# Optimization experiments

Measured on AMD Instinct MI355X. Metric: run time of the kernel, lower is better.

The kernel has to match this reference:

```python
import jax, jax.numpy as jnp
import numpy as np

K = 16          # k_neighbours
BIG = 1e9       # distance penalty for masked senders


def setup_inputs() -> dict:
    key = jax.random.key(0)
    ks = jax.random.split(key, 8)
    B, N, F, H, FO = 64, 512, 64, 128, 64
    nodes = jax.random.normal(ks[0], (B, N, F), jnp.float32)
    mask = jax.random.randint(ks[1], (B, N), 0, 2, jnp.int32)

    def w(k_, sh):
        return jax.random.normal(k_, sh, jnp.float32) * (1.0 / np.sqrt(sh[0]).astype(np.float32))

    We1 = w(ks[2], (2 * F, H)); be1 = jnp.zeros((H,), jnp.float32)
    We2 = w(ks[3], (H, H));     be2 = jnp.zeros((H,), jnp.float32)
    Wn1 = w(ks[4], (F + H, H)); bn1 = jnp.zeros((H,), jnp.float32)
    Wn2 = w(ks[5], (H, FO));    bn2 = jnp.zeros((FO,), jnp.float32)
    return dict(nodes=nodes, mask=mask, We1=We1, be1=be1, We2=We2, be2=be2,
                Wn1=Wn1, bn1=bn1, Wn2=Wn2, bn2=bn2)


def reference(nodes, mask, We1, be1, We2, be2, Wn1, bn1, Wn2, bn2):
    # nodes: [B,N,F] ; mask: [B,N] (1 = real node, 0 = padding)
    m = mask.astype(nodes.dtype)                      # [B,N]
    x = nodes * m[..., None]                          # zero padded nodes

    # --- dynamic kNN graph (euclidean_squared + top_k, no self connection) ---
    sq = jnp.sum(x * x, axis=-1)                      # [B,N]
    dist = jnp.abs(sq[:, :, None] + sq[:, None, :]
                   - 2.0 * jnp.einsum('bnf,bmf->bnm', x, x))  # [B,N,N]
    dist = dist + BIG * (1.0 - m)[:, None, :]         # never select masked senders
    _, idx = jax.lax.top_k(-dist, K + 1)              # [B,N,K+1]
    idx = idx[..., 1:]                                # drop self connection -> [B,N,K]

    # --- gather sender features / masks along edges ---
    gathered = jax.vmap(lambda xf, ib: xf[ib])(x, idx)    # [B,N,K,F]
    smask = jax.vmap(lambda mv, ib: mv[ib])(m, idx)       # [B,N,K]
    recv = jnp.broadcast_to(x[:, :, None, :], gathered.shape)
    edges = jnp.concatenate([recv, gathered], axis=-1)    # [B,N,K,2F] ('concat' aggregation)

    # --- edge MLP (gather-compute) ---
    h = jax.nn.relu(edges @ We1 + be1)
    h = jax.nn.relu(h @ We2 + be2)                        # [B,N,K,H]

    # --- masked mean pooling over edges (scatter back to nodes) ---
    emask = m[:, :, None] * smask                         # edge valid iff both endpoints valid
    h = h * emask[..., None]
    cnt = jnp.maximum(jnp.sum(emask, axis=-1, keepdims=True), 1.0)  # [B,N,1]
    pooled = jnp.sum(h, axis=2) / cnt                     # [B,N,H]

    # --- node update MLP ---
    nh = jnp.concatenate([x, pooled], axis=-1)            # [B,N,F+H]
    out = jax.nn.relu(nh @ Wn1 + bn1) @ Wn2 + bn2         # [B,N,FO]
    return out * m[..., None]                             # zero padded nodes in output
```

## Files before the change

### kernel.cpp

```cpp
#include <hip/hip_runtime.h>

#define DI __device__ __forceinline__

typedef __bf16 bf16_t;
typedef __bf16 bf16x4 __attribute__((ext_vector_type(4)));
typedef __bf16 bf16x8 __attribute__((ext_vector_type(8)));
typedef float f32x4 __attribute__((ext_vector_type(4)));
typedef unsigned long long u64;


DI bf16_t f2b(float f) {
  unsigned u = __float_as_uint(f);
  unsigned r = (u + 0x7fffu + ((u >> 16) & 1u)) >> 16;
  return __builtin_bit_cast(bf16_t, (unsigned short)r);
}
DI float b2f(bf16_t h) {
  return __uint_as_float(((unsigned)__builtin_bit_cast(unsigned short, h)) << 16);
}
DI f32x4 zero4() { f32x4 z = {0.f, 0.f, 0.f, 0.f}; return z; }

DI bf16x8 make_frag(const float* p, bool wantlo) {
  float4 v0 = *(const float4*)p;
  float4 v1 = *(const float4*)(p + 4);
  float vv[8] = {v0.x, v0.y, v0.z, v0.w, v1.x, v1.y, v1.z, v1.w};
  bf16x8 a;
#pragma unroll
  for (int j = 0; j < 8; ++j) {
    bf16_t hi = f2b(vv[j]);
    a[j] = wantlo ? f2b(vv[j] - b2f(hi)) : hi;
  }
  return a;
}

DI u64 u64min(u64 a, u64 b) { return a < b ? a : b; }
template <int CTRL>
DI u64 dpp_u64(u64 v) {
  int lo = (int)(unsigned)(v & 0xffffffffull);
  int hi = (int)(unsigned)(v >> 32);
  int tlo = __builtin_amdgcn_update_dpp(0, lo, CTRL, 0xF, 0xF, true);
  int thi = __builtin_amdgcn_update_dpp(0, hi, CTRL, 0xF, 0xF, true);
  return (((u64)(unsigned)thi) << 32) | (unsigned)tlo;
}
template <int CTRL>
DI float dpp_f32(float v) {
  int t = __builtin_amdgcn_update_dpp(0, (int)__float_as_uint(v), CTRL, 0xF, 0xF, true);
  return __uint_as_float((unsigned)t);
}
DI u64 rowmin_u64(u64 v) {
  v = u64min(v, dpp_u64<0xB1>(v));
  v = u64min(v, dpp_u64<0x4E>(v));
  v = u64min(v, dpp_u64<0x141>(v));
  v = u64min(v, dpp_u64<0x140>(v));
  return v;
}
DI float rowsum_f32(float v) {
  v += dpp_f32<0xB1>(v);
  v += dpp_f32<0x4E>(v);
  v += dpp_f32<0x141>(v);
  v += dpp_f32<0x140>(v);
  return v;
}
DI void bitonic16(u64* a) {
#pragma unroll
  for (int k = 2; k <= 16; k <<= 1)
#pragma unroll
    for (int j = k >> 1; j > 0; j >>= 1)
#pragma unroll
      for (int i = 0; i < 16; ++i) {
        const int l = i ^ j;
        if (l > i) {
          const bool up = ((i & k) == 0);
          const bool sw = up ? (a[i] > a[l]) : (a[i] < a[l]);
          const u64 t0 = a[i], t1 = a[l];
          a[i] = sw ? t1 : t0;
          a[l] = sw ? t0 : t1;
        }
      }
}

__global__ void __launch_bounds__(256) kfuse(const float* __restrict__ nodes,
    const int* __restrict__ mask,
    const float* __restrict__ We1, const float* __restrict__ We2,
    const float* __restrict__ Wn1, const float* __restrict__ Wn2,
    float* __restrict__ x, bf16_t* __restrict__ xhi, bf16_t* __restrict__ xlo,
    float* __restrict__ sq, int* __restrict__ vlist, int* __restrict__ vcnt,
    bf16_t* __restrict__ W1p, bf16_t* __restrict__ W2p,
    bf16_t* __restrict__ Wn1p, bf16_t* __restrict__ Wn2p) {
  const int blk = blockIdx.x, t = threadIdx.x;
  __shared__ int cnts[8];
  __shared__ int basep[8];

  if (blk < 512) {
    const int b = blk >> 3, n0 = (blk & 7) * 64;
#pragma unroll
    for (int i = 0; i < 4; ++i) {
      const int idx = t + 256 * i;
      const int gi = b * 512 + n0 + (idx >> 4);
      const int fo = (idx & 15) * 4;
      const float fm = (float)mask[gi];
      const size_t ro = (size_t)gi * 64;
      float4 v = *(const float4*)(nodes + ro + fo);
      v.x *= fm; v.y *= fm; v.z *= fm; v.w *= fm;
      *(float4*)(x + ro + fo) = v;
      float vv[4] = {v.x, v.y, v.z, v.w};
      bf16x4 hh, ll;
#pragma unroll
      for (int k = 0; k < 4; ++k) {
        bf16_t hi = f2b(vv[k]);
        hh[k] = hi;
        ll[k] = f2b(vv[k] - b2f(hi));
      }
      *(bf16x4*)(xhi + ro + fo) = hh;
      *(bf16x4*)(xlo + ro + fo) = ll;
      float s = v.x * v.x + v.y * v.y + v.z * v.z + v.w * v.w;
      s = rowsum_f32(s);
      if ((t & 15) == 0) sq[gi] = s;
    }
  } else if (blk < 576) {
    const int b = blk - 512, lane = t & 63, w = t >> 6;
    unsigned long long bal[2]; int flag[2];
#pragma unroll
    for (int h = 0; h < 2; ++h) {
      flag[h] = (mask[b * 512 + h * 256 + t] != 0);
      bal[h] = __ballot(flag[h]);
      if (lane == 0) cnts[h * 4 + w] = __popcll(bal[h]);
    }
    __syncthreads();
    if (t == 0) {
      int a = 0;
      for (int c = 0; c < 8; ++c) { basep[c] = a; a += cnts[c]; }
      vcnt[b] = a;
    }
    __syncthreads();
#pragma unroll
    for (int h = 0; h < 2; ++h) {
      if (flag[h]) {
        const unsigned long long lt = (lane == 0) ? 0ull : (~0ull >> (64 - lane));
        const int pos = basep[h * 4 + w] + __popcll(bal[h] & lt);
        vlist[b * 512 + pos] = h * 256 + t;
      }
    }
  } else {
    int p = (blk - 576) * 256 + t;
    const float* W; bf16_t* dst; int K, Nn, local, mode;
    if (p < 4096)       { W = We1; dst = W1p;  K = 128; Nn = 128; mode = 0; local = p; }
    else if (p < 8192)  { W = We2; dst = W2p;  K = 128; Nn = 128; mode = 1; local = p - 4096; }
    else if (p < 14336) { W = Wn1; dst = Wn1p; K = 192; Nn = 128; mode = 0; local = p - 8192; }
    else                { W = Wn2; dst = Wn2p; K = 128; Nn = 64;  mode = 1; local = p - 14336; }
    int lane = local & 63;
    int nnt = (Nn >> 4);
    int chunk = local >> 6;
    int nt = chunk % nnt;
    int s = chunk / nnt;
    int n = nt * 16 + (lane & 15);
    int kbase = s * 32 + ((lane >> 4) * 8);
    bf16x8 v;
#pragma unroll
    for (int j = 0; j < 8; ++j) {
      int kp = kbase + j;
      int region = kp / K;
      int kk = kp - region * K;
      float w = W[kk * Nn + n];
      bf16_t hi = f2b(w);
      v[j] = (mode == 1 && region == 1) ? f2b(w - b2f(hi)) : hi;
    }
    *(bf16x8*)(dst + (size_t)local * 8) = v;
  }
}

__global__ void __launch_bounds__(256) kknn(const bf16_t* __restrict__ xhi,
    const bf16_t* __restrict__ xlo,
    const float* __restrict__ sq, const int* __restrict__ vlist,
    const int* __restrict__ vcnt, int* __restrict__ idxg) {
  const int b = blockIdx.x & 63, tile = blockIdx.x >> 6;
  const int nv = vcnt[b];
  if (tile * 16 >= nv) return;
  const int t = threadIdx.x, lane = t & 63, w = t >> 6;
  const int i = lane >> 4, d = lane & 15;
  __shared__ float sqs[512];
  __shared__ int vls[512];
  __shared__ __align__(16) float S[16 * 520];
  for (int k = t; k < 512; k += 256) { sqs[k] = sq[b * 512 + k]; vls[k] = vlist[b * 512 + k]; }
  __syncthreads();

  const size_t xb = (size_t)b * 512 * 64;

  const int aslot = tile * 16 + d;
  const int arow = vls[aslot < nv ? aslot : 0];
  bf16x8 ah[2], al[2];
#pragma unroll
  for (int kh = 0; kh < 2; ++kh) {
    ah[kh] = *(const bf16x8*)(xhi + xb + (size_t)arow * 64 + kh * 32 + i * 8);
    al[kh] = *(const bf16x8*)(xlo + xb + (size_t)arow * 64 + kh * 32 + i * 8);
  }

  const int rslot = tile * 16 + w * 4 + i;
  const bool vrow = (rslot < nv);
  const int nrow = vls[rslot < nv ? rslot : 0];
  const float sqn = sqs[nrow];

  int crs[8];
#pragma unroll
  for (int jj = 0; jj < 8; ++jj) {
    const int c = (w + 4 * jj) * 16 + d;
    crs[jj] = vls[c < nv ? c : 0];
  }

  bf16x8 bh[2], bl[2];
  if (w * 16 < nv) {
#pragma unroll
    for (int kh = 0; kh < 2; ++kh) {
      bh[kh] = *(const bf16x8*)(xhi + xb + (size_t)crs[0] * 64 + kh * 32 + i * 8);
      bl[kh] = *(const bf16x8*)(xlo + xb + (size_t)crs[0] * 64 + kh * 32 + i * 8);
    }
  }
  for (int jj = 0; jj < 8; ++jj) {
    const int ct = w + 4 * jj;
    if (ct * 16 >= nv) break;
    bf16x8 nbh[2], nbl[2];
    const bool pre = (jj < 7) && ((w + 4 * (jj + 1)) * 16 < nv);
    if (pre) {
#pragma unroll
      for (int kh = 0; kh < 2; ++kh) {
        nbh[kh] = *(const bf16x8*)(xhi + xb + (size_t)crs[jj + 1] * 64 + kh * 32 + i * 8);
        nbl[kh] = *(const bf16x8*)(xlo + xb + (size_t)crs[jj + 1] * 64 + kh * 32 + i * 8);
      }
    }
    f32x4 acc = zero4();
#pragma unroll
    for (int kh = 0; kh < 2; ++kh) {
      acc = __builtin_amdgcn_mfma_f32_16x16x32_bf16(ah[kh], bh[kh], acc, 0, 0, 0);
      acc = __builtin_amdgcn_mfma_f32_16x16x32_bf16(ah[kh], bl[kh], acc, 0, 0, 0);
      acc = __builtin_amdgcn_mfma_f32_16x16x32_bf16(al[kh], bh[kh], acc, 0, 0, 0);
      acc = __builtin_amdgcn_mfma_f32_16x16x32_bf16(al[kh], bl[kh], acc, 0, 0, 0);
    }
#pragma unroll
    for (int r = 0; r < 4; ++r) S[(i * 4 + r) * 520 + ct * 16 + d] = acc[r];
    if (pre) {
#pragma unroll
      for (int kh = 0; kh < 2; ++kh) { bh[kh] = nbh[kh]; bl[kh] = nbl[kh]; }
    }
  }
  __syncthreads();

  const u64 INF64 = ~0ull;
  u64 s1[16], s2[16];
#pragma unroll
  for (int j = 0; j < 16; ++j) { s1[j] = INF64; s2[j] = INF64; }
#pragma unroll
  for (int j = 0; j < 32; ++j) {
    if (j * 16 < nv) {
      const int c = j * 16 + d;
      const int m = vls[c < nv ? c : 0];
      const float dot = S[(w * 4 + i) * 520 + j * 16 + d];
      const float dd = fabsf(sqn + sqs[m] - 2.f * dot);
      const u64 key = (((u64)__float_as_uint(dd)) << 32) | (unsigned)m;
      const bool ok = (c < nv) && (m != nrow);
      if (j < 16) s1[j] = ok ? key : INF64;
      else        s2[j - 16] = ok ? key : INF64;
    }
  }
  bitonic16(s1);
  const bool two = (nv > 256);
  if (two) bitonic16(s2);

  int res = nrow;
#pragma unroll
  for (int ts = 0; ts < 16; ++ts) {
    const u64 head = two ? u64min(s1[0], s2[0]) : s1[0];
    const u64 wmin = rowmin_u64(head);
    if (d == ts) res = (wmin == INF64) ? nrow : (int)(unsigned)(wmin & 0xffffffffull);
    const bool w1 = (wmin != INF64) && (s1[0] == wmin);
#pragma unroll
    for (int k = 0; k < 15; ++k) s1[k] = w1 ? s1[k + 1] : s1[k];
    s1[15] = w1 ? INF64 : s1[15];
    if (two) {
      const bool w2 = (wmin != INF64) && (s2[0] == wmin);
#pragma unroll
      for (int k = 0; k < 15; ++k) s2[k] = w2 ? s2[k + 1] : s2[k];
      s2[15] = w2 ? INF64 : s2[15];
    }
  }
  if (vrow) idxg[((size_t)b * 512 + rslot) * 16 + d] = res;
}

__global__ void __launch_bounds__(256, 2) kedge(const bf16_t* __restrict__ xhi,
    const bf16_t* __restrict__ xlo, const int* __restrict__ idxg,
    const int* __restrict__ vlist, const int* __restrict__ vcnt,
    const bf16_t* __restrict__ W1p, const bf16_t* __restrict__ W2p,
    const float* __restrict__ be1, const float* __restrict__ be2,
    float* __restrict__ pooled) {
  __shared__ __align__(16) bf16_t wbuf[32768];
  __shared__ __align__(16) bf16_t hfrag[4][2][1024];
  const int t = threadIdx.x, lane = t & 63, w = t >> 6;
  const int q = lane >> 4, e = lane & 15;
  const int bb = blockIdx.x & 63;
  const int s0 = ((blockIdx.x >> 6) * 4 + w) * 2;

  {
    const uint4* s1 = (const uint4*)W1p;
    const uint4* s2 = (const uint4*)W2p;
    uint4* dst = (uint4*)wbuf;
#pragma unroll
    for (int i = 0; i < 8; ++i) dst[t + 256 * i] = s1[t + 256 * i];
#pragma unroll
    for (int i = 0; i < 8; ++i) dst[2048 + t + 256 * i] = s2[t + 256 * i];
  }
  __syncthreads();

  const int nv = vcnt[bb];
  if (s0 >= nv) return;

  int vl[2], sv[2];
  {
#pragma unroll
    for (int u = 0; u < 2; ++u) {
      const int sl = (s0 + u) < nv ? (s0 + u) : 0;
      vl[u] = vlist[bb * 512 + sl];
      sv[u] = idxg[((size_t)(bb * 512 + sl) << 4) + e];
    }
  }

  for (int base = s0; base < nv; base += 64) {
    const bool act1 = (base + 1) < nv;
    const int gid0 = bb * 512 + vl[0];
    const int gid1 = bb * 512 + vl[1];
    const size_t rb0 = (size_t)gid0 << 6;
    const size_t rb1 = (size_t)gid1 << 6;
    const size_t nb0 = (size_t)(bb * 512 + sv[0]) << 6;
    const size_t nb1 = (size_t)(bb * 512 + sv[1]) << 6;

    bf16x8 af[2][8];
#pragma unroll
    for (int k = 0; k < 4; ++k) {
      const int off = (k & 1) * 32 + q * 8;
      const bf16_t* pl = (k >> 1) ? xlo : xhi;
      af[0][k]     = *(const bf16x8*)(pl + rb0 + off);
      af[1][k]     = *(const bf16x8*)(pl + rb1 + off);
      af[0][4 + k] = *(const bf16x8*)(pl + nb0 + off);
      af[1][4 + k] = *(const bf16x8*)(pl + nb1 + off);
    }

    int nvl[2] = {vl[0], vl[1]}, nsv[2] = {sv[0], sv[1]};
    {
      const int nb = base + 64;
      if (nb < nv) {
#pragma unroll
        for (int u = 0; u < 2; ++u) {
          const int sl = (nb + u) < nv ? (nb + u) : 0;
          nvl[u] = vlist[bb * 512 + sl];
          nsv[u] = idxg[((size_t)(bb * 512 + sl) << 4) + e];
        }
      }
    }

    f32x4 acc[2][8];
#pragma unroll
    for (int u = 0; u < 2; ++u)
#pragma unroll
      for (int nt = 0; nt < 8; ++nt) acc[u][nt] = zero4();

#pragma unroll
    for (int ph = 0; ph < 2; ++ph)
#pragma unroll
      for (int k = 0; k < 4; ++k) {
        const bf16_t* wb = wbuf + (ph * 2 + (k & 1)) * 4096;
        const bf16x8 a0 = af[0][ph * 4 + k];
        const bf16x8 a1 = af[1][ph * 4 + k];
#pragma unroll
        for (int nt = 0; nt < 8; ++nt) {
          const bf16x8 bfv = *(const bf16x8*)(wb + (nt * 64 + lane) * 8);
          acc[0][nt] = __builtin_amdgcn_mfma_f32_16x16x32_bf16(a0, bfv, acc[0][nt], 0, 0, 0);
          acc[1][nt] = __builtin_amdgcn_mfma_f32_16x16x32_bf16(a1, bfv, acc[1][nt], 0, 0, 0);
        }
      }

    f32x4 acc2[2][8];
#pragma unroll
    for (int u = 0; u < 2; ++u)
#pragma unroll
      for (int nt = 0; nt < 8; ++nt) acc2[u][nt] = zero4();

#pragma unroll
    for (int hh = 0; hh < 2; ++hh) {
#pragma unroll
      for (int u = 0; u < 2; ++u)
#pragma unroll
        for (int nt4 = 0; nt4 < 4; ++nt4) {
          const int nt = hh * 4 + nt4;
          const int cc = nt * 16 + e;
          const float bv = be1[cc];
          const int bse = (((cc >> 5) & 1) * 64 + q * 4 + 16 * ((cc >> 3) & 3)) * 8 + (cc & 7);
#pragma unroll
          for (int r = 0; r < 4; ++r)
            hfrag[w][u][bse + r * 8] = f2b(fmaxf(acc[u][nt][r] + bv, 0.f));
        }
#pragma unroll
      for (int sl = 0; sl < 2; ++sl) {
        const int f = hh * 2 + sl;
        const bf16x8 a20 = *(const bf16x8*)(&hfrag[w][0][(sl * 64 + lane) * 8]);
        const bf16x8 a21 = *(const bf16x8*)(&hfrag[w][1][(sl * 64 + lane) * 8]);
        const bf16_t* wb2 = wbuf + 16384 + f * 4096;
#pragma unroll
        for (int nt = 0; nt < 8; ++nt) {
          const bf16x8 bfv = *(const bf16x8*)(wb2 + (nt * 64 + lane) * 8);
          acc2[0][nt] = __builtin_amdgcn_mfma_f32_16x16x32_bf16(a20, bfv, acc2[0][nt], 0, 0, 0);
          acc2[1][nt] = __builtin_amdgcn_mfma_f32_16x16x32_bf16(a21, bfv, acc2[1][nt], 0, 0, 0);
        }
      }
    }

#pragma unroll
    for (int u = 0; u < 2; ++u) {
      if (u == 0 || act1) {
        const int gid = u ? gid1 : gid0;
#pragma unroll
        for (int nt = 0; nt < 8; ++nt) {
          const float bv = be2[nt * 16 + e];
          float part = 0.f;
#pragma unroll
          for (int r = 0; r < 4; ++r) part += fmaxf(acc2[u][nt][r] + bv, 0.f);
          part += __shfl_xor(part, 16, 64);
          part += __shfl_xor(part, 32, 64);
          if (lane < 16) pooled[(size_t)gid * 128 + nt * 16 + lane] = part * 0.0625f;
        }
      }
    }

    vl[0] = nvl[0]; vl[1] = nvl[1];
    sv[0] = nsv[0]; sv[1] = nsv[1];
  }
}

__global__ void __launch_bounds__(256) knode(const float* __restrict__ x,
    const float* __restrict__ pooled, const int* __restrict__ mask,
    const bf16_t* __restrict__ Wn1p, const bf16_t* __restrict__ Wn2p,
    const float* __restrict__ bn1, const float* __restrict__ bn2,
    float* __restrict__ out) {
  __shared__ __align__(16) bf16_t wbuf[8192];
  __shared__ __align__(16) bf16_t hfrag[4][2][2048];
  const int t = threadIdx.x, lane = t & 63, w = t >> 6;
  const int q = lane >> 4, e = lane & 15;
  int nodebase[2];
#pragma unroll
  for (int u = 0; u < 2; ++u) nodebase[u] = (blockIdx.x * 8 + w * 2 + u) * 16;

  f32x4 acc[2][8];
#pragma unroll
  for (int u = 0; u < 2; ++u)
#pragma unroll
    for (int nt = 0; nt < 8; ++nt) acc[u][nt] = zero4();

#pragma unroll
  for (int ph = 0; ph < 3; ++ph) {
    __syncthreads();
    {
      const uint4* src = (const uint4*)(Wn1p + (size_t)ph * 8192);
      uint4* dst = (uint4*)wbuf;
#pragma unroll
      for (int i = 0; i < 4; ++i) dst[t + 256 * i] = src[t + 256 * i];
    }
    __syncthreads();
#pragma unroll
    for (int k = 0; k < 4; ++k) {
      const int s = 2 * ph + (k & 1) + (k >> 1) * 6;
      const bool wantlo = (s >= 6);
      const int sr = wantlo ? (s - 6) : s;
      const int col = sr * 32 + q * 8;
      bf16x8 af[2];
#pragma unroll
      for (int u = 0; u < 2; ++u) {
        const int node = nodebase[u] + e;
        const float* p = (col < 64) ? (x + (size_t)node * 64 + col)
                                    : (pooled + (size_t)node * 128 + (col - 64));
        af[u] = make_frag(p, wantlo);
      }
      const int bslab = s & 1;
#pragma unroll
      for (int nt = 0; nt < 8; ++nt) {
        const bf16x8 bfv = *(const bf16x8*)(wbuf + bslab * 4096 + (nt * 64 + lane) * 8);
#pragma unroll
        for (int u = 0; u < 2; ++u)
          acc[u][nt] = __builtin_amdgcn_mfma_f32_16x16x32_bf16(af[u], bfv, acc[u][nt], 0, 0, 0);
      }
    }
  }

#pragma unroll
  for (int u = 0; u < 2; ++u) {
#pragma unroll
    for (int nt = 0; nt < 8; ++nt) {
      const int cc = nt * 16 + e;
      const float bv = bn1[cc];
      const int base = ((cc >> 5) * 64 + (q * 4) + 16 * ((cc >> 3) & 3)) * 8 + (cc & 7);
#pragma unroll
      for (int r = 0; r < 4; ++r) {
        float h = fmaxf(acc[u][nt][r] + bv, 0.f);
        hfrag[w][u][base + r * 8] = f2b(h);
      }
    }
  }

  f32x4 acc2[2][4];
#pragma unroll
  for (int u = 0; u < 2; ++u)
#pragma unroll
    for (int nt = 0; nt < 4; ++nt) acc2[u][nt] = zero4();

  __syncthreads();
  {
    const uint4* src = (const uint4*)Wn2p;
    uint4* dst = (uint4*)wbuf;
#pragma unroll
    for (int i = 0; i < 4; ++i) dst[t + 256 * i] = src[t + 256 * i];
  }
  __syncthreads();
#pragma unroll
  for (int sl = 0; sl < 4; ++sl) {
    bf16x8 af[2];
#pragma unroll
    for (int u = 0; u < 2; ++u)
      af[u] = *(const bf16x8*)(&hfrag[w][u][(sl * 64 + lane) * 8]);
#pragma unroll
    for (int nt = 0; nt < 4; ++nt) {
      const bf16x8 bfv = *(const bf16x8*)(wbuf + sl * 2048 + (nt * 64 + lane) * 8);
#pragma unroll
      for (int u = 0; u < 2; ++u)
        acc2[u][nt] = __builtin_amdgcn_mfma_f32_16x16x32_bf16(af[u], bfv, acc2[u][nt], 0, 0, 0);
    }
  }

#pragma unroll
  for (int u = 0; u < 2; ++u) {
    int mm[4];
#pragma unroll
    for (int r = 0; r < 4; ++r) mm[r] = mask[nodebase[u] + q * 4 + r];
#pragma unroll
    for (int nt = 0; nt < 4; ++nt) {
      const float bv = bn2[nt * 16 + e];
#pragma unroll
      for (int r = 0; r < 4; ++r) {
        const int node = nodebase[u] + q * 4 + r;
        out[(size_t)node * 64 + nt * 16 + e] = (acc2[u][nt][r] + bv) * (float)mm[r];
      }
    }
  }
}

extern "C" void kernel_launch(void* const* d_in, const int* in_sizes, int n_in,
                              void* d_out, int out_size, void* d_ws, size_t ws_size,
                              hipStream_t stream) {
  const float* nodes = (const float*)d_in[0];
  const int*   mask  = (const int*)d_in[1];
  const float* We1   = (const float*)d_in[2];
  const float* be1   = (const float*)d_in[3];
  const float* We2   = (const float*)d_in[4];
  const float* be2   = (const float*)d_in[5];
  const float* Wn1   = (const float*)d_in[6];
  const float* bn1   = (const float*)d_in[7];
  const float* Wn2   = (const float*)d_in[8];
  const float* bn2   = (const float*)d_in[9];
  float* out = (float*)d_out;

  char* p = (char*)d_ws;
  auto alloc = [&](size_t bytes) -> char* {
    char* r = p;
    p += (bytes + 255) & ~(size_t)255;
    return r;
  };
  float*  x      = (float*)alloc((size_t)32768 * 64 * 4);
  bf16_t* xhi    = (bf16_t*)alloc((size_t)32768 * 64 * 2);
  bf16_t* xlo    = (bf16_t*)alloc((size_t)32768 * 64 * 2);
  float*  sq     = (float*)alloc((size_t)32768 * 4);
  int*    vlist  = (int*)alloc((size_t)32768 * 4);
  int*    vcnt   = (int*)alloc((size_t)64 * 4);
  int*    idxg   = (int*)alloc((size_t)32768 * 16 * 4);
  float*  pooled = (float*)alloc((size_t)32768 * 128 * 4);
  bf16_t* W1p    = (bf16_t*)alloc((size_t)8 * 8 * 64 * 8 * 2);
  bf16_t* W2p    = (bf16_t*)alloc((size_t)8 * 8 * 64 * 8 * 2);
  bf16_t* Wn1p   = (bf16_t*)alloc((size_t)12 * 8 * 64 * 8 * 2);
  bf16_t* Wn2p   = (bf16_t*)alloc((size_t)8 * 4 * 64 * 8 * 2);
  if ((size_t)(p - (char*)d_ws) > ws_size) return;

  kfuse<<<640, 256, 0, stream>>>(nodes, mask, We1, We2, Wn1, Wn2,
                                 x, xhi, xlo, sq, vlist, vcnt, W1p, W2p, Wn1p, Wn2p);
  kknn<<<2048, 256, 0, stream>>>(xhi, xlo, sq, vlist, vcnt, idxg);
  kedge<<<512, 256, 0, stream>>>(xhi, xlo, idxg, vlist, vcnt, W1p, W2p, be1, be2, pooled);
  knode<<<256, 256, 0, stream>>>(x, pooled, mask, Wn1p, Wn2p, bn1, bn2, out);
}
```

Baseline: 166.6 us.

## Restructure node MLP kernel: one tile per wave, weights loaded once, 512 blocks

The node-update kernel now processes one 16-node tile per wave instead of two, and launches twice as many blocks so more CUs get work. All Wn1 and Wn2 weights are staged into shared memory in a single pass, which removes the per-phase reload-and-sync loop. The second GEMM is interleaved with the hidden-layer write-back in two halves, which shrinks the hfrag buffer. In exchange, each block uses more LDS (about 72 KB), which may limit how many blocks fit per CU, and every block still reloads the full weight set.

```diff
diff --git a/kernel.cpp b/kernel.cpp
--- a/kernel.cpp
+++ b/kernel.cpp
@@ -432,117 +432,90 @@
   }
 }
 
-__global__ void __launch_bounds__(256) knode(const float* __restrict__ x,
+__global__ void __launch_bounds__(256, 2) knode(const float* __restrict__ x,
     const float* __restrict__ pooled, const int* __restrict__ mask,
     const bf16_t* __restrict__ Wn1p, const bf16_t* __restrict__ Wn2p,
     const float* __restrict__ bn1, const float* __restrict__ bn2,
     float* __restrict__ out) {
-  __shared__ __align__(16) bf16_t wbuf[8192];
-  __shared__ __align__(16) bf16_t hfrag[4][2][2048];
+  __shared__ __align__(16) bf16_t wbuf[32768];
+  __shared__ __align__(16) bf16_t hfrag[4][1024];
   const int t = threadIdx.x, lane = t & 63, w = t >> 6;
   const int q = lane >> 4, e = lane & 15;
-  int nodebase[2];
-#pragma unroll
-  for (int u = 0; u < 2; ++u) nodebase[u] = (blockIdx.x * 8 + w * 2 + u) * 16;
-
-  f32x4 acc[2][8];
-#pragma unroll
-  for (int u = 0; u < 2; ++u)
-#pragma unroll
-    for (int nt = 0; nt < 8; ++nt) acc[u][nt] = zero4();
-
-#pragma unroll
-  for (int ph = 0; ph < 3; ++ph) {
-    __syncthreads();
-    {
-      const uint4* src = (const uint4*)(Wn1p + (size_t)ph * 8192);
-      uint4* dst = (uint4*)wbuf;
-#pragma unroll
-      for (int i = 0; i < 4; ++i) dst[t + 256 * i] = src[t + 256 * i];
-    }
-    __syncthreads();
+  const int nodebase = (blockIdx.x * 4 + w) * 16;
+
+  {
+    const uint4* s1 = (const uint4*)Wn1p;
+    const uint4* s2 = (const uint4*)Wn2p;
+    uint4* dst = (uint4*)wbuf;
+#pragma unroll
+    for (int i = 0; i < 12; ++i) dst[t + 256 * i] = s1[t + 256 * i];
+#pragma unroll
+    for (int i = 0; i < 4; ++i) dst[3072 + t + 256 * i] = s2[t + 256 * i];
+  }
+  __syncthreads();
+
+  f32x4 acc[8];
+#pragma unroll
+  for (int nt = 0; nt < 8; ++nt) acc[nt] = zero4();
+
+#pragma unroll
+  for (int ph = 0; ph < 3; ++ph)
 #pragma unroll
     for (int k = 0; k < 4; ++k) {
       const int s = 2 * ph + (k & 1) + (k >> 1) * 6;
       const bool wantlo = (s >= 6);
       const int sr = wantlo ? (s - 6) : s;
       const int col = sr * 32 + q * 8;
-      bf16x8 af[2];
-#pragma unroll
-      for (int u = 0; u < 2; ++u) {
-        const int node = nodebase[u] + e;
-        const float* p = (col < 64) ? (x + (size_t)node * 64 + col)
-                                    : (pooled + (size_t)node * 128 + (col - 64));
-        af[u] = make_frag(p, wantlo);
-      }
-      const int bslab = s & 1;
+      const int node = nodebase + e;
+      const float* p = (col < 64) ? (x + (size_t)node * 64 + col)
+                                  : (pooled + (size_t)node * 128 + (col - 64));
+      const bf16x8 af = make_frag(p, wantlo);
 #pragma unroll
       for (int nt = 0; nt < 8; ++nt) {
-        const bf16x8 bfv = *(const bf16x8*)(wbuf + bslab * 4096 + (nt * 64 + lane) * 8);
-#pragma unroll
-        for (int u = 0; u < 2; ++u)
-          acc[u][nt] = __builtin_amdgcn_mfma_f32_16x16x32_bf16(af[u], bfv, acc[u][nt], 0, 0, 0);
-      }
-    }
-  }
-
-#pragma unroll
-  for (int u = 0; u < 2; ++u) {
-#pragma unroll
-    for (int nt = 0; nt < 8; ++nt) {
+        const bf16x8 bfv = *(const bf16x8*)(wbuf + sr * 4096 + (nt * 64 + lane) * 8);
+        acc[nt] = __builtin_amdgcn_mfma_f32_16x16x32_bf16(af, bfv, acc[nt], 0, 0, 0);
+      }
+    }
+
+  f32x4 acc2[4];
+#pragma unroll
+  for (int nt = 0; nt < 4; ++nt) acc2[nt] = zero4();
+
+#pragma unroll
+  for (int hh = 0; hh < 2; ++hh) {
+#pragma unroll
+    for (int nt4 = 0; nt4 < 4; ++nt4) {
+      const int nt = hh * 4 + nt4;
       const int cc = nt * 16 + e;
       const float bv = bn1[cc];
-      const int base = ((cc >> 5) * 64 + (q * 4) + 16 * ((cc >> 3) & 3)) * 8 + (cc & 7);
-#pragma unroll
-      for (int r = 0; r < 4; ++r) {
-        float h = fmaxf(acc[u][nt][r] + bv, 0.f);
-        hfrag[w][u][base + r * 8] = f2b(h);
-      }
-    }
-  }
-
-  f32x4 acc2[2][4];
-#pragma unroll
-  for (int u = 0; u < 2; ++u)
-#pragma unroll
-    for (int nt = 0; nt < 4; ++nt) acc2[u][nt] = zero4();
-
-  __syncthreads();
-  {
-    const uint4* src = (const uint4*)Wn2p;
-    uint4* dst = (uint4*)wbuf;
-#pragma unroll
-    for (int i = 0; i < 4; ++i) dst[t + 256 * i] = src[t + 256 * i];
-  }
-  __syncthreads();
-#pragma unroll
-  for (int sl = 0; sl < 4; ++sl) {
-    bf16x8 af[2];
-#pragma unroll
-    for (int u = 0; u < 2; ++u)
-      af[u] = *(const bf16x8*)(&hfrag[w][u][(sl * 64 + lane) * 8]);
-#pragma unroll
-    for (int nt = 0; nt < 4; ++nt) {
-      const bf16x8 bfv = *(const bf16x8*)(wbuf + sl * 2048 + (nt * 64 + lane) * 8);
-#pragma unroll
-      for (int u = 0; u < 2; ++u)
-        acc2[u][nt] = __builtin_amdgcn_mfma_f32_16x16x32_bf16(af[u], bfv, acc2[u][nt], 0, 0, 0);
-    }
-  }
-
-#pragma unroll
-  for (int u = 0; u < 2; ++u) {
-    int mm[4];
-#pragma unroll
-    for (int r = 0; r < 4; ++r) mm[r] = mask[nodebase[u] + q * 4 + r];
-#pragma unroll
-    for (int nt = 0; nt < 4; ++nt) {
-      const float bv = bn2[nt * 16 + e];
-#pragma unroll
-      for (int r = 0; r < 4; ++r) {
-        const int node = nodebase[u] + q * 4 + r;
-        out[(size_t)node * 64 + nt * 16 + e] = (acc2[u][nt][r] + bv) * (float)mm[r];
-      }
+      const int bse = (((cc >> 5) & 1) * 64 + q * 4 + 16 * ((cc >> 3) & 3)) * 8 + (cc & 7);
+#pragma unroll
+      for (int r = 0; r < 4; ++r)
+        hfrag[w][bse + r * 8] = f2b(fmaxf(acc[nt][r] + bv, 0.f));
+    }
+#pragma unroll
+    for (int sl = 0; sl < 2; ++sl) {
+      const int f = hh * 2 + sl;
+      const bf16x8 a2 = *(const bf16x8*)(&hfrag[w][(sl * 64 + lane) * 8]);
+      const bf16_t* wb2 = wbuf + 24576 + f * 2048;
+#pragma unroll
+      for (int nt = 0; nt < 4; ++nt) {
+        const bf16x8 bfv = *(const bf16x8*)(wb2 + (nt * 64 + lane) * 8);
+        acc2[nt] = __builtin_amdgcn_mfma_f32_16x16x32_bf16(a2, bfv, acc2[nt], 0, 0, 0);
+      }
+    }
+  }
+
+  int mm[4];
+#pragma unroll
+  for (int r = 0; r < 4; ++r) mm[r] = mask[nodebase + q * 4 + r];
+#pragma unroll
+  for (int nt = 0; nt < 4; ++nt) {
+    const float bv = bn2[nt * 16 + e];
+#pragma unroll
+    for (int r = 0; r < 4; ++r) {
+      const int node = nodebase + q * 4 + r;
+      out[(size_t)node * 64 + nt * 16 + e] = (acc2[nt][r] + bv) * (float)mm[r];
     }
   }
 }
@@ -586,5 +559,5 @@
                                  x, xhi, xlo, sq, vlist, vcnt, W1p, W2p, Wn1p, Wn2p);
   kknn<<<2048, 256, 0, stream>>>(xhi, xlo, sq, vlist, vcnt, idxg);
   kedge<<<512, 256, 0, stream>>>(xhi, xlo, idxg, vlist, vcnt, W1p, W2p, be1, be2, pooled);
-  knode<<<256, 256, 0, stream>>>(x, pooled, mask, Wn1p, Wn2p, bn1, bn2, out);
-}
+  knode<<<512, 256, 0, stream>>>(x, pooled, mask, Wn1p, Wn2p, bn1, bn2, out);
+}
```

Measured after the change: 163.6 us. Within noise of the previous version (-1.8%).
